# Performance work log

Hardware: AMD Instinct MI355X
Metric: run time of the kernel (lower is better)

The kernel has to match this reference:

```python
import jax, jax.numpy as jnp
import numpy as np

# --- config constants (from init_kwargs) ---
ALPHA = 0.05; SIGMA = 0.2; THETA = 0.3; A = 0.02; B_PAR = 0.1; RHO = 0.5
MULT = 2.0          # config.x_range_final[1]
GAMMA = 0.5         # power-utility exponent: u(x,r)=r*x^g/g, ux=r*x^(g-1)
N_STEPS = 100; T_FINAL = 1.0; DT = T_FINAL / N_STEPS
HID = 64; BATCH = 16384
PEN_SCALE = 100.0; LOWER = 1e-6


def _mlp(W1, b1, W2, b2, W3, b3, s):
    # tiny FeedForwardSubNet: 3 -> HID -> HID -> 1, tanh activations
    h = jnp.tanh(s @ W1 + b1)
    h = jnp.tanh(h @ W2 + b2)
    return h @ W3 + b3


def _penalise(v):
    # penalise_range(v, lower): quadratic hinge below `lower`
    return PEN_SCALE * jnp.square(jnp.maximum(LOWER - v, 0.0))


def setup_inputs() -> dict:
    key = jax.random.key(0)
    ks = jax.random.split(key, 16)
    dw = jax.random.normal(ks[0], (BATCH, 1, N_STEPS), dtype=jnp.float32) * float(np.sqrt(DT))
    X0 = jnp.ones((1,), jnp.float32)
    R0 = jnp.ones((1,), jnp.float32)
    def w(k, shape, fan):
        return jax.random.normal(k, shape, jnp.float32) / np.float32(np.sqrt(fan))
    inp = {"dw": dw, "X0": X0, "R0": R0,
           "pW1": w(ks[1], (3, HID), 3), "pb1": jnp.zeros((HID,), jnp.float32),
           "pW2": w(ks[2], (HID, HID), HID), "pb2": jnp.zeros((HID,), jnp.float32),
           "pW3": w(ks[3], (HID, 1), HID), "pb3": jnp.zeros((1,), jnp.float32),
           "qW1": w(ks[4], (3, HID), 3), "qb1": jnp.zeros((HID,), jnp.float32),
           "qW2": w(ks[5], (HID, HID), HID), "qb2": jnp.zeros((HID,), jnp.float32),
           "qW3": w(ks[6], (HID, 1), HID), "qb3": jnp.zeros((1,), jnp.float32)}
    return inp


def reference(dw, X0, R0, pW1, pb1, pW2, pb2, pW3, pb3, qW1, qb1, qW2, qb2, qW3, qb3):
    Bn = dw.shape[0]
    ones = jnp.ones((Bn, 1), dw.dtype)
    times = jnp.arange(N_STEPS + 1, dtype=dw.dtype) * DT   # [N+1]
    x0 = ones * X0
    R0v = ones * R0
    b_eff = float(np.sign(RHO)) * B_PAR

    # p_0 and dp_0 = d p_0 / d x (per-sample, rowwise independent net)
    def p_of_x(xx):
        st = jnp.concatenate([MULT * times[0] * ones, xx, R0v], 1)
        return _mlp(pW1, pb1, pW2, pb2, pW3, pb3, st)
    p0, p_vjp = jax.vjp(p_of_x, x0)
    (dp0,) = p_vjp(jnp.ones_like(p0))
    pi0 = _mlp(qW1, qb1, qW2, qb2, qW3, qb3,
               jnp.concatenate([MULT * times[0] * ones, x0, R0v], 1))

    dw_t = jnp.transpose(dw, (2, 0, 1))          # [N, B, 1]
    upd = jnp.arange(N_STEPS) < (N_STEPS - 1)    # pi not updated at last step

    def step(carry, inp):
        x, min_x, W, pi = carry
        dwi, t_next, u = inp
        x = x + x * ALPHA * DT + pi * SIGMA * THETA * DT + pi * SIGMA * dwi
        min_x = jnp.minimum(x, min_x)
        W = W + dwi
        Rv = R0v * jnp.exp((A - 0.5 * b_eff ** 2) * t_next + b_eff * W)
        p = p0 * jnp.exp(-(ALPHA + 0.5 * THETA ** 2) * t_next - THETA * W)
        st = jnp.concatenate([MULT * t_next * jnp.ones_like(x), x, Rv], 1)
        pi_new = _mlp(qW1, qb1, qW2, qb2, qW3, qb3, st)
        pi = jnp.where(u, pi_new, pi)
        return (x, min_x, W, pi), (x, Rv, pi, -p)

    (xf, min_x, Wf, pif), (xs, Rs, pis, dMs) = jax.lax.scan(
        step, (x0, x0, jnp.zeros_like(x0), pi0), (dw_t, times[1:], upd))

    # stacked process data, matching tf.concat-over-axis-0 ordering: [(N+1)*B, 1]
    x_all  = jnp.concatenate([x0[None], xs], 0).reshape(-1, 1)
    r_all  = jnp.concatenate([R0v[None], Rs], 0).reshape(-1, 1)
    pi_all = jnp.concatenate([pi0[None], pis], 0).reshape(-1, 1)
    dM_all = jnp.concatenate([(-p0)[None], dMs], 0).reshape(-1, 1)
    dM2_all = jnp.tile(-dp0, (N_STEPS + 1, 1))
    proc = jnp.concatenate([x_all, r_all, pi_all, dM_all, dM2_all], 1)  # [(N+1)*B, 5]

    # losses (non_concave = False branch)
    p_fin = -dMs[-1]
    R_fin = Rs[-1]
    xc = jnp.maximum(xf, LOWER)
    ux = R_fin * xc ** (GAMMA - 1.0)
    u_val = R_fin * xc ** GAMMA / GAMMA
    pen = _penalise(min_x)
    loss_p = jnp.mean(jnp.square(p_fin + ux) + pen)
    loss_pi = loss_p + jnp.mean(-u_val + pen)

    return jnp.concatenate([proc.reshape(-1), jnp.stack([loss_p, loss_pi])])
```

## Files before the change

### kernel.cpp

```cpp
#include <hip/hip_runtime.h>
#include <hip/hip_bf16.h>
#include <math.h>

#define NSTEP 100
#define BATCH 16384
#define MB 16
#define NBLK (BATCH/MB)
#define NT 64

#define C_ALPHA 0.05f
#define C_SIGMA 0.2f
#define C_THETA 0.3f
#define C_DT    0.01f
#define C_LOWER 1e-6f
#define C_PEN   100.0f
#define LOG2E   1.4426950408889634f
#define TSCALE  (2.0f * LOG2E)
#define CRT ( 0.015f * C_DT * LOG2E)
#define CRW ( 0.1f * LOG2E)
#define CPT (-0.095f * C_DT * LOG2E)
#define CPW (-0.3f * LOG2E)

typedef __attribute__((ext_vector_type(8))) short bf16x8;
typedef __attribute__((ext_vector_type(4))) float f32x4;

__device__ __forceinline__ float tanh_pre(float zs) {
    float e = __builtin_amdgcn_exp2f(zs);
    return 1.0f - 2.0f * __builtin_amdgcn_rcpf(e + 1.0f);
}
__device__ __forceinline__ unsigned f2bf_u(float f) {
    unsigned u = __float_as_uint(f);
    return (u + 0x7FFFu + ((u >> 16) & 1u)) >> 16;
}
__device__ __forceinline__ unsigned pack_bf16(float a, float b) {
    union { __hip_bfloat162 h; unsigned u; } cv;
    cv.h = __float22bfloat162_rn(make_float2(a, b));
    return cv.u;
}
__device__ __forceinline__ float dpp_row_sum16(float v) {
    int t;
    t = __builtin_amdgcn_update_dpp(0, __float_as_int(v), 0x128, 0xF, 0xF, true);
    v += __int_as_float(t);
    t = __builtin_amdgcn_update_dpp(0, __float_as_int(v), 0x124, 0xF, 0xF, true);
    v += __int_as_float(t);
    t = __builtin_amdgcn_update_dpp(0, __float_as_int(v), 0x122, 0xF, 0xF, true);
    v += __int_as_float(t);
    t = __builtin_amdgcn_update_dpp(0, __float_as_int(v), 0x121, 0xF, 0xF, true);
    v += __int_as_float(t);
    return v;
}

__global__ __launch_bounds__(NT, 1) void fused_kernel(
        const float* __restrict__ dw, const float* __restrict__ X0,
        const float* __restrict__ R0,
        const float* __restrict__ pW1, const float* __restrict__ pb1,
        const float* __restrict__ pW2, const float* __restrict__ pb2,
        const float* __restrict__ pW3, const float* __restrict__ pb3,
        const float* __restrict__ qW1, const float* __restrict__ qb1,
        const float* __restrict__ qW2, const float* __restrict__ qb2,
        const float* __restrict__ qW3, const float* __restrict__ qb3,
        float* __restrict__ ws, float* __restrict__ out) {
    __shared__ __align__(16) unsigned short sW2T[64 * 72];
    __shared__ __align__(16) float sdw[MB * NSTEP];

    const int lane = threadIdx.x;
    const int b0 = blockIdx.x * MB;
    const int l15 = lane & 15, quad = lane >> 4;

    {
        const float4* g = (const float4*)(dw + (size_t)b0 * NSTEP);
        float4* s = (float4*)sdw;
        #pragma unroll
        for (int u = lane; u < MB * NSTEP / 4; u += NT) s[u] = g[u];
    }
    #pragma unroll 8
    for (int t = 0; t < 64; t++)
        sW2T[lane * 72 + t] = (unsigned short)f2bf_u(qW2[t * 64 + lane] * TSCALE);
    __syncthreads();

    bf16x8 Bf[4][2];
    #pragma unroll
    for (int nt = 0; nt < 4; nt++) {
        const unsigned short* r = &sW2T[(nt * 16 + l15) * 72 + quad * 8];
        Bf[nt][0] = *(const bf16x8*)r;
        Bf[nt][1] = *(const bf16x8*)(r + 32);
    }
    float tco[16], w1xs[16], w1rs[16], b1s[16];
    #pragma unroll
    for (int idx = 0; idx < 16; idx++) {
        int k = (idx < 8) ? (quad * 8 + idx) : (32 + quad * 8 + (idx - 8));
        tco[idx]  = qW1[k] * (2.0f * C_DT * TSCALE);
        w1xs[idx] = qW1[64 + k] * TSCALE;
        w1rs[idx] = qW1[128 + k] * TSCALE;
        b1s[idx]  = qb1[k] * TSCALE;
    }
    float b2v[4], w3v[4];
    #pragma unroll
    for (int nt = 0; nt < 4; nt++) {
        b2v[nt] = qb2[nt * 16 + l15] * TSCALE;
        w3v[nt] = qW3[nt * 16 + l15];
    }
    const float b3 = qb3[0];
    const float X0v = X0[0], R0s = R0[0];
    const int bperm_idx = (((l15 >> 2) * 16) + (l15 & 3)) * 4;

    float p0, dp0;
    {
        float pre = fmaf(pW1[64 + lane], X0v, fmaf(pW1[128 + lane], R0s, pb1[lane]));
        float h1 = tanh_pre(TSCALE * pre);
        float d1 = (1.0f - h1 * h1) * pW1[64 + lane];
        float a0 = pb2[lane], a1 = 0.f, a2 = 0.f, a3 = 0.f;
        float e0 = 0.f, e1 = 0.f, e2 = 0.f, e3 = 0.f;
        for (int i2 = 0; i2 < 64; i2 += 4) {
            float w0 = pW2[(i2 + 0) * 64 + lane];
            float w1 = pW2[(i2 + 1) * 64 + lane];
            float w2 = pW2[(i2 + 2) * 64 + lane];
            float w3 = pW2[(i2 + 3) * 64 + lane];
            a0 = fmaf(__shfl(h1, i2 + 0), w0, a0); e0 = fmaf(__shfl(d1, i2 + 0), w0, e0);
            a1 = fmaf(__shfl(h1, i2 + 1), w1, a1); e1 = fmaf(__shfl(d1, i2 + 1), w1, e1);
            a2 = fmaf(__shfl(h1, i2 + 2), w2, a2); e2 = fmaf(__shfl(d1, i2 + 2), w2, e2);
            a3 = fmaf(__shfl(h1, i2 + 3), w3, a3); e3 = fmaf(__shfl(d1, i2 + 3), w3, e3);
        }
        float pre2 = (a0 + a1) + (a2 + a3);
        float dpre2 = (e0 + e1) + (e2 + e3);
        float h2 = tanh_pre(TSCALE * pre2);
        float d2 = (1.0f - h2 * h2) * dpre2;
        float c1 = h2 * pW3[lane], c2 = d2 * pW3[lane];
        #pragma unroll
        for (int o = 1; o < 64; o <<= 1) {
            c1 += __shfl_xor(c1, o);
            c2 += __shfl_xor(c2, o);
        }
        p0 = c1 + pb3[0]; dp0 = c2;
    }

    auto qnet = [&](float fi, float xv, float rv) -> float {
        union { bf16x8 v; unsigned u[4]; } A0, A1;
        #pragma unroll
        for (int p = 0; p < 8; p++) {
            const int i0 = 2 * p, i1 = 2 * p + 1;
            float z0 = fmaf(w1rs[i0], rv, fmaf(w1xs[i0], xv, fmaf(tco[i0], fi, b1s[i0])));
            float z1 = fmaf(w1rs[i1], rv, fmaf(w1xs[i1], xv, fmaf(tco[i1], fi, b1s[i1])));
            unsigned pk = pack_bf16(tanh_pre(z0), tanh_pre(z1));
            if (p < 4) A0.u[p] = pk; else A1.u[p - 4] = pk;
        }
        f32x4 acc0 = {b2v[0], b2v[0], b2v[0], b2v[0]};
        f32x4 acc1 = {b2v[1], b2v[1], b2v[1], b2v[1]};
        f32x4 acc2 = {b2v[2], b2v[2], b2v[2], b2v[2]};
        f32x4 acc3 = {b2v[3], b2v[3], b2v[3], b2v[3]};
        acc0 = __builtin_amdgcn_mfma_f32_16x16x32_bf16(A0.v, Bf[0][0], acc0, 0, 0, 0);
        acc1 = __builtin_amdgcn_mfma_f32_16x16x32_bf16(A0.v, Bf[1][0], acc1, 0, 0, 0);
        acc2 = __builtin_amdgcn_mfma_f32_16x16x32_bf16(A0.v, Bf[2][0], acc2, 0, 0, 0);
        acc3 = __builtin_amdgcn_mfma_f32_16x16x32_bf16(A0.v, Bf[3][0], acc3, 0, 0, 0);
        acc0 = __builtin_amdgcn_mfma_f32_16x16x32_bf16(A1.v, Bf[0][1], acc0, 0, 0, 0);
        acc1 = __builtin_amdgcn_mfma_f32_16x16x32_bf16(A1.v, Bf[1][1], acc1, 0, 0, 0);
        acc2 = __builtin_amdgcn_mfma_f32_16x16x32_bf16(A1.v, Bf[2][1], acc2, 0, 0, 0);
        acc3 = __builtin_amdgcn_mfma_f32_16x16x32_bf16(A1.v, Bf[3][1], acc3, 0, 0, 0);
        f32x4 part;
        #pragma unroll
        for (int r = 0; r < 4; r++) {
            float sA = fmaf(tanh_pre(acc1[r]), w3v[1], tanh_pre(acc0[r]) * w3v[0]);
            float sB = fmaf(tanh_pre(acc3[r]), w3v[3], tanh_pre(acc2[r]) * w3v[2]);
            part[r] = dpp_row_sum16(sA + sB);
        }
        float sLo = (lane & 1) ? part[1] : part[0];
        float sHi = (lane & 1) ? part[3] : part[2];
        float sel = (lane & 2) ? sHi : sLo;
        int g = __builtin_amdgcn_ds_bpermute(bperm_idx, __float_as_int(sel));
        return __int_as_float(g) + b3;
    };

    float x = X0v, Wsum = 0.0f, minx = X0v;
    float pi = qnet(0.0f, X0v, R0s);
    if (quad == 0) {
        size_t base = (size_t)(b0 + l15) * 5;
        out[base] = X0v; out[base + 1] = R0s; out[base + 2] = pi;
        out[base + 3] = -p0; out[base + 4] = -dp0;
    }

    float dw_next = sdw[l15 * NSTEP];
    #pragma unroll 1
    for (int i = 0; i < NSTEP - 1; i++) {
        const float fi = (float)(i + 1);
        float dwv = dw_next;
        dw_next = sdw[l15 * NSTEP + i + 1];
        float t = pi * C_SIGMA;
        x = fmaf(x, 1.0f + C_ALPHA * C_DT, fmaf(t, dwv, t * (C_THETA * C_DT)));
        minx = fminf(minx, x);
        Wsum += dwv;
        float R = R0s * __builtin_amdgcn_exp2f(fmaf(CRW, Wsum, CRT * fi));
        float pm = p0 * __builtin_amdgcn_exp2f(fmaf(CPW, Wsum, CPT * fi));
        float pin = qnet(fi, x, R);
        if (quad == 0) {
            size_t base = ((size_t)(i + 1) * BATCH + b0 + l15) * 5;
            out[base] = x; out[base + 1] = R; out[base + 2] = pin;
            out[base + 3] = -pm; out[base + 4] = -dp0;
        }
        pi = pin;
    }

    {
        float dwv = dw_next;
        float t = pi * C_SIGMA;
        x = fmaf(x, 1.0f + C_ALPHA * C_DT, fmaf(t, dwv, t * (C_THETA * C_DT)));
        minx = fminf(minx, x);
        Wsum += dwv;
        float Rf = R0s * __builtin_amdgcn_exp2f(fmaf(CRW, Wsum, CRT * (float)NSTEP));
        float pf = p0 * __builtin_amdgcn_exp2f(fmaf(CPW, Wsum, CPT * (float)NSTEP));
        if (quad == 0) {
            size_t base = ((size_t)NSTEP * BATCH + b0 + l15) * 5;
            out[base] = x; out[base + 1] = Rf; out[base + 2] = pi;
            out[base + 3] = -pf; out[base + 4] = -dp0;
        }
        float xc = fmaxf(x, C_LOWER);
        float ux = Rf * rsqrtf(xc);
        float uval = 2.0f * Rf * sqrtf(xc);
        float d = fmaxf(C_LOWER - minx, 0.0f);
        float pen = C_PEN * d * d;
        float t1 = pf + ux;
        float v1 = dpp_row_sum16(t1 * t1 + pen);
        float v2 = dpp_row_sum16(-uval + pen);
        if (lane == 0) {
            atomicAdd(&ws[3], v1);
            atomicAdd(&ws[4], v2);
            __threadfence();
            int old = atomicAdd((int*)(ws + 5), 1);
            if (old == NBLK - 1) {
                float lp = atomicAdd(&ws[3], 0.0f) * (1.0f / (float)BATCH);
                float lq = atomicAdd(&ws[4], 0.0f) * (1.0f / (float)BATCH);
                out[(size_t)(NSTEP + 1) * BATCH * 5] = lp;
                out[(size_t)(NSTEP + 1) * BATCH * 5 + 1] = lp + lq;
            }
        }
    }
}

extern "C" void kernel_launch(void* const* d_in, const int* in_sizes, int n_in,
                              void* d_out, int out_size, void* d_ws, size_t ws_size,
                              hipStream_t stream) {
    const float* dw  = (const float*)d_in[0];
    const float* X0  = (const float*)d_in[1];
    const float* R0  = (const float*)d_in[2];
    const float* pW1 = (const float*)d_in[3];
    const float* pb1 = (const float*)d_in[4];
    const float* pW2 = (const float*)d_in[5];
    const float* pb2 = (const float*)d_in[6];
    const float* pW3 = (const float*)d_in[7];
    const float* pb3 = (const float*)d_in[8];
    const float* qW1 = (const float*)d_in[9];
    const float* qb1 = (const float*)d_in[10];
    const float* qW2 = (const float*)d_in[11];
    const float* qb2 = (const float*)d_in[12];
    const float* qW3 = (const float*)d_in[13];
    const float* qb3 = (const float*)d_in[14];
    float* out = (float*)d_out;
    float* ws  = (float*)d_ws;

    hipMemsetAsync(d_ws, 0, 64, stream);
    fused_kernel<<<NBLK, NT, 0, stream>>>(dw, X0, R0, pW1, pb1, pW2, pb2, pW3, pb3,
                                          qW1, qb1, qW2, qb2, qW3, qb3, ws, out);
}
```

Measured before the change: 209.6 us.

## Split each block's q-net hidden units across two waves with LDS exchange

```diff
diff --git a/kernel.cpp b/kernel.cpp
--- a/kernel.cpp
+++ b/kernel.cpp
@@ -6,7 +6,7 @@
 #define BATCH 16384
 #define MB 16
 #define NBLK (BATCH/MB)
-#define NT 64
+#define NT 128
 
 #define C_ALPHA 0.05f
 #define C_SIGMA 0.2f
@@ -50,7 +50,7 @@
     return v;
 }
 
-__global__ __launch_bounds__(NT, 1) void fused_kernel(
+__global__ __launch_bounds__(NT, 2) void fused_kernel(
         const float* __restrict__ dw, const float* __restrict__ X0,
         const float* __restrict__ R0,
         const float* __restrict__ pW1, const float* __restrict__ pb1,
@@ -62,8 +62,12 @@
         float* __restrict__ ws, float* __restrict__ out) {
     __shared__ __align__(16) unsigned short sW2T[64 * 72];
     __shared__ __align__(16) float sdw[MB * NSTEP];
-
-    const int lane = threadIdx.x;
+    __shared__ __align__(16) uint4 sA[2][2][64];
+    __shared__ __align__(16) float sP[2][2][16];
+
+    const int tid = threadIdx.x;
+    const int lane = tid & 63;
+    const int wv = tid >> 6;
     const int b0 = blockIdx.x * MB;
     const int l15 = lane & 15, quad = lane >> 4;
 
@@ -71,38 +75,38 @@
         const float4* g = (const float4*)(dw + (size_t)b0 * NSTEP);
         float4* s = (float4*)sdw;
         #pragma unroll
-        for (int u = lane; u < MB * NSTEP / 4; u += NT) s[u] = g[u];
-    }
-    #pragma unroll 8
-    for (int t = 0; t < 64; t++)
-        sW2T[lane * 72 + t] = (unsigned short)f2bf_u(qW2[t * 64 + lane] * TSCALE);
+        for (int u = tid; u < MB * NSTEP / 4; u += NT) s[u] = g[u];
+    }
+    for (int u = tid; u < 4096; u += NT) {
+        int k = u >> 6, n = u & 63;
+        sW2T[n * 72 + k] = (unsigned short)f2bf_u(qW2[u] * TSCALE);
+    }
     __syncthreads();
 
-    bf16x8 Bf[4][2];
+    bf16x8 Bf[2][2];
     #pragma unroll
-    for (int nt = 0; nt < 4; nt++) {
-        const unsigned short* r = &sW2T[(nt * 16 + l15) * 72 + quad * 8];
-        Bf[nt][0] = *(const bf16x8*)r;
-        Bf[nt][1] = *(const bf16x8*)(r + 32);
-    }
-    float tco[16], w1xs[16], w1rs[16], b1s[16];
+    for (int t = 0; t < 2; t++) {
+        const unsigned short* r = &sW2T[(wv * 32 + t * 16 + l15) * 72 + quad * 8];
+        Bf[t][0] = *(const bf16x8*)r;
+        Bf[t][1] = *(const bf16x8*)(r + 32);
+    }
+    float tco[8], w1xs[8], w1rs[8], b1s[8];
     #pragma unroll
-    for (int idx = 0; idx < 16; idx++) {
-        int k = (idx < 8) ? (quad * 8 + idx) : (32 + quad * 8 + (idx - 8));
-        tco[idx]  = qW1[k] * (2.0f * C_DT * TSCALE);
-        w1xs[idx] = qW1[64 + k] * TSCALE;
-        w1rs[idx] = qW1[128 + k] * TSCALE;
-        b1s[idx]  = qb1[k] * TSCALE;
-    }
-    float b2v[4], w3v[4];
+    for (int j = 0; j < 8; j++) {
+        int k = wv * 32 + quad * 8 + j;
+        tco[j]  = qW1[k] * (2.0f * C_DT * TSCALE);
+        w1xs[j] = qW1[64 + k] * TSCALE;
+        w1rs[j] = qW1[128 + k] * TSCALE;
+        b1s[j]  = qb1[k] * TSCALE;
+    }
+    float b2v[2], w3v[2];
     #pragma unroll
-    for (int nt = 0; nt < 4; nt++) {
-        b2v[nt] = qb2[nt * 16 + l15] * TSCALE;
-        w3v[nt] = qW3[nt * 16 + l15];
+    for (int t = 0; t < 2; t++) {
+        b2v[t] = qb2[wv * 32 + t * 16 + l15] * TSCALE;
+        w3v[t] = qW3[wv * 32 + t * 16 + l15];
     }
     const float b3 = qb3[0];
     const float X0v = X0[0], R0s = R0[0];
-    const int bperm_idx = (((l15 >> 2) * 16) + (l15 & 3)) * 4;
 
     float p0, dp0;
     {
@@ -134,45 +138,39 @@
         p0 = c1 + pb3[0]; dp0 = c2;
     }
 
-    auto qnet = [&](float fi, float xv, float rv) -> float {
-        union { bf16x8 v; unsigned u[4]; } A0, A1;
-        #pragma unroll
-        for (int p = 0; p < 8; p++) {
+    auto qnet = [&](int par, float fi, float xv, float rv) -> float {
+        union { uint4 u4; bf16x8 v; unsigned u[4]; } Aloc, Aoth;
+        #pragma unroll
+        for (int p = 0; p < 4; p++) {
             const int i0 = 2 * p, i1 = 2 * p + 1;
             float z0 = fmaf(w1rs[i0], rv, fmaf(w1xs[i0], xv, fmaf(tco[i0], fi, b1s[i0])));
             float z1 = fmaf(w1rs[i1], rv, fmaf(w1xs[i1], xv, fmaf(tco[i1], fi, b1s[i1])));
-            unsigned pk = pack_bf16(tanh_pre(z0), tanh_pre(z1));
-            if (p < 4) A0.u[p] = pk; else A1.u[p - 4] = pk;
-        }
+            Aloc.u[p] = pack_bf16(tanh_pre(z0), tanh_pre(z1));
+        }
+        sA[par][wv][lane] = Aloc.u4;
+        __syncthreads();
+        Aoth.u4 = sA[par][1 - wv][lane];
+        bf16x8 A0 = (wv == 0) ? Aloc.v : Aoth.v;
+        bf16x8 A1 = (wv == 0) ? Aoth.v : Aloc.v;
         f32x4 acc0 = {b2v[0], b2v[0], b2v[0], b2v[0]};
         f32x4 acc1 = {b2v[1], b2v[1], b2v[1], b2v[1]};
-        f32x4 acc2 = {b2v[2], b2v[2], b2v[2], b2v[2]};
-        f32x4 acc3 = {b2v[3], b2v[3], b2v[3], b2v[3]};
-        acc0 = __builtin_amdgcn_mfma_f32_16x16x32_bf16(A0.v, Bf[0][0], acc0, 0, 0, 0);
-        acc1 = __builtin_amdgcn_mfma_f32_16x16x32_bf16(A0.v, Bf[1][0], acc1, 0, 0, 0);
-        acc2 = __builtin_amdgcn_mfma_f32_16x16x32_bf16(A0.v, Bf[2][0], acc2, 0, 0, 0);
-        acc3 = __builtin_amdgcn_mfma_f32_16x16x32_bf16(A0.v, Bf[3][0], acc3, 0, 0, 0);
-        acc0 = __builtin_amdgcn_mfma_f32_16x16x32_bf16(A1.v, Bf[0][1], acc0, 0, 0, 0);
-        acc1 = __builtin_amdgcn_mfma_f32_16x16x32_bf16(A1.v, Bf[1][1], acc1, 0, 0, 0);
-        acc2 = __builtin_amdgcn_mfma_f32_16x16x32_bf16(A1.v, Bf[2][1], acc2, 0, 0, 0);
-        acc3 = __builtin_amdgcn_mfma_f32_16x16x32_bf16(A1.v, Bf[3][1], acc3, 0, 0, 0);
+        acc0 = __builtin_amdgcn_mfma_f32_16x16x32_bf16(A0, Bf[0][0], acc0, 0, 0, 0);
+        acc1 = __builtin_amdgcn_mfma_f32_16x16x32_bf16(A0, Bf[1][0], acc1, 0, 0, 0);
+        acc0 = __builtin_amdgcn_mfma_f32_16x16x32_bf16(A1, Bf[0][1], acc0, 0, 0, 0);
+        acc1 = __builtin_amdgcn_mfma_f32_16x16x32_bf16(A1, Bf[1][1], acc1, 0, 0, 0);
         f32x4 part;
         #pragma unroll
-        for (int r = 0; r < 4; r++) {
-            float sA = fmaf(tanh_pre(acc1[r]), w3v[1], tanh_pre(acc0[r]) * w3v[0]);
-            float sB = fmaf(tanh_pre(acc3[r]), w3v[3], tanh_pre(acc2[r]) * w3v[2]);
-            part[r] = dpp_row_sum16(sA + sB);
-        }
-        float sLo = (lane & 1) ? part[1] : part[0];
-        float sHi = (lane & 1) ? part[3] : part[2];
-        float sel = (lane & 2) ? sHi : sLo;
-        int g = __builtin_amdgcn_ds_bpermute(bperm_idx, __float_as_int(sel));
-        return __int_as_float(g) + b3;
+        for (int r = 0; r < 4; r++)
+            part[r] = dpp_row_sum16(
+                fmaf(tanh_pre(acc1[r]), w3v[1], tanh_pre(acc0[r]) * w3v[0]));
+        if (l15 == 0) *(f32x4*)&sP[par][wv][quad * 4] = part;
+        __syncthreads();
+        return sP[par][0][l15] + sP[par][1][l15] + b3;
     };
 
     float x = X0v, Wsum = 0.0f, minx = X0v;
-    float pi = qnet(0.0f, X0v, R0s);
-    if (quad == 0) {
+    float pi = qnet(0, 0.0f, X0v, R0s);
+    if (wv == 1 && quad == 0) {
         size_t base = (size_t)(b0 + l15) * 5;
         out[base] = X0v; out[base + 1] = R0s; out[base + 2] = pi;
         out[base + 3] = -p0; out[base + 4] = -dp0;
@@ -190,8 +188,8 @@
         Wsum += dwv;
         float R = R0s * __builtin_amdgcn_exp2f(fmaf(CRW, Wsum, CRT * fi));
         float pm = p0 * __builtin_amdgcn_exp2f(fmaf(CPW, Wsum, CPT * fi));
-        float pin = qnet(fi, x, R);
-        if (quad == 0) {
+        float pin = qnet((i + 1) & 1, fi, x, R);
+        if (wv == 1 && quad == 0) {
             size_t base = ((size_t)(i + 1) * BATCH + b0 + l15) * 5;
             out[base] = x; out[base + 1] = R; out[base + 2] = pin;
             out[base + 3] = -pm; out[base + 4] = -dp0;
@@ -207,29 +205,31 @@
         Wsum += dwv;
         float Rf = R0s * __builtin_amdgcn_exp2f(fmaf(CRW, Wsum, CRT * (float)NSTEP));
         float pf = p0 * __builtin_amdgcn_exp2f(fmaf(CPW, Wsum, CPT * (float)NSTEP));
-        if (quad == 0) {
+        if (wv == 1 && quad == 0) {
             size_t base = ((size_t)NSTEP * BATCH + b0 + l15) * 5;
             out[base] = x; out[base + 1] = Rf; out[base + 2] = pi;
             out[base + 3] = -pf; out[base + 4] = -dp0;
         }
-        float xc = fmaxf(x, C_LOWER);
-        float ux = Rf * rsqrtf(xc);
-        float uval = 2.0f * Rf * sqrtf(xc);
-        float d = fmaxf(C_LOWER - minx, 0.0f);
-        float pen = C_PEN * d * d;
-        float t1 = pf + ux;
-        float v1 = dpp_row_sum16(t1 * t1 + pen);
-        float v2 = dpp_row_sum16(-uval + pen);
-        if (lane == 0) {
-            atomicAdd(&ws[3], v1);
-            atomicAdd(&ws[4], v2);
-            __threadfence();
-            int old = atomicAdd((int*)(ws + 5), 1);
-            if (old == NBLK - 1) {
-                float lp = atomicAdd(&ws[3], 0.0f) * (1.0f / (float)BATCH);
-                float lq = atomicAdd(&ws[4], 0.0f) * (1.0f / (float)BATCH);
-                out[(size_t)(NSTEP + 1) * BATCH * 5] = lp;
-                out[(size_t)(NSTEP + 1) * BATCH * 5 + 1] = lp + lq;
+        if (wv == 0) {
+            float xc = fmaxf(x, C_LOWER);
+            float ux = Rf * rsqrtf(xc);
+            float uval = 2.0f * Rf * sqrtf(xc);
+            float d = fmaxf(C_LOWER - minx, 0.0f);
+            float pen = C_PEN * d * d;
+            float t1 = pf + ux;
+            float v1 = dpp_row_sum16(t1 * t1 + pen);
+            float v2 = dpp_row_sum16(-uval + pen);
+            if (lane == 0) {
+                atomicAdd(&ws[3], v1);
+                atomicAdd(&ws[4], v2);
+                __threadfence();
+                int old = atomicAdd((int*)(ws + 5), 1);
+                if (old == NBLK - 1) {
+                    float lp = atomicAdd(&ws[3], 0.0f) * (1.0f / (float)BATCH);
+                    float lq = atomicAdd(&ws[4], 0.0f) * (1.0f / (float)BATCH);
+                    out[(size_t)(NSTEP + 1) * BATCH * 5] = lp;
+                    out[(size_t)(NSTEP + 1) * BATCH * 5 + 1] = lp + lq;
+                }
             }
         }
     }
```

Result: no change. 208.9 us (-0.3%).

## Precompute R and p paths off the serial loop and shorten per-step dependency chain

Applied to the files above, without the earlier changes.

```diff
diff --git a/kernel.cpp b/kernel.cpp
--- a/kernel.cpp
+++ b/kernel.cpp
@@ -20,6 +20,7 @@
 #define CRW ( 0.1f * LOG2E)
 #define CPT (-0.095f * C_DT * LOG2E)
 #define CPW (-0.3f * LOG2E)
+#define XMUL (1.0f + C_ALPHA * C_DT)
 
 typedef __attribute__((ext_vector_type(8))) short bf16x8;
 typedef __attribute__((ext_vector_type(4))) float f32x4;
@@ -62,6 +63,8 @@
         float* __restrict__ ws, float* __restrict__ out) {
     __shared__ __align__(16) unsigned short sW2T[64 * 72];
     __shared__ __align__(16) float sdw[MB * NSTEP];
+    __shared__ __align__(16) float sR[NSTEP * MB];
+    __shared__ float sPf[MB];
 
     const int lane = threadIdx.x;
     const int b0 = blockIdx.x * MB;
@@ -78,31 +81,8 @@
         sW2T[lane * 72 + t] = (unsigned short)f2bf_u(qW2[t * 64 + lane] * TSCALE);
     __syncthreads();
 
-    bf16x8 Bf[4][2];
-    #pragma unroll
-    for (int nt = 0; nt < 4; nt++) {
-        const unsigned short* r = &sW2T[(nt * 16 + l15) * 72 + quad * 8];
-        Bf[nt][0] = *(const bf16x8*)r;
-        Bf[nt][1] = *(const bf16x8*)(r + 32);
-    }
-    float tco[16], w1xs[16], w1rs[16], b1s[16];
-    #pragma unroll
-    for (int idx = 0; idx < 16; idx++) {
-        int k = (idx < 8) ? (quad * 8 + idx) : (32 + quad * 8 + (idx - 8));
-        tco[idx]  = qW1[k] * (2.0f * C_DT * TSCALE);
-        w1xs[idx] = qW1[64 + k] * TSCALE;
-        w1rs[idx] = qW1[128 + k] * TSCALE;
-        b1s[idx]  = qb1[k] * TSCALE;
-    }
-    float b2v[4], w3v[4];
-    #pragma unroll
-    for (int nt = 0; nt < 4; nt++) {
-        b2v[nt] = qb2[nt * 16 + l15] * TSCALE;
-        w3v[nt] = qW3[nt * 16 + l15];
-    }
+    const float X0v = X0[0], R0s = R0[0];
     const float b3 = qb3[0];
-    const float X0v = X0[0], R0s = R0[0];
-    const int bperm_idx = (((l15 >> 2) * 16) + (l15 & 3)) * 4;
 
     float p0, dp0;
     {
@@ -134,34 +114,91 @@
         p0 = c1 + pb3[0]; dp0 = c2;
     }
 
-    auto qnet = [&](float fi, float xv, float rv) -> float {
-        union { bf16x8 v; unsigned u[4]; } A0, A1;
-        #pragma unroll
-        for (int p = 0; p < 8; p++) {
-            const int i0 = 2 * p, i1 = 2 * p + 1;
-            float z0 = fmaf(w1rs[i0], rv, fmaf(w1xs[i0], xv, fmaf(tco[i0], fi, b1s[i0])));
-            float z1 = fmaf(w1rs[i1], rv, fmaf(w1xs[i1], xv, fmaf(tco[i1], fi, b1s[i1])));
-            unsigned pk = pack_bf16(tanh_pre(z0), tanh_pre(z1));
-            if (p < 4) A0.u[p] = pk; else A1.u[p - 4] = pk;
-        }
+    {
+        const int ps = lane >> 2;
+        const int pc = lane & 3;
+        float loc = 0.0f;
+        #pragma unroll 5
+        for (int j = pc * 25; j < pc * 25 + 25; j++) loc += sdw[ps * NSTEP + j];
+        float o0 = __shfl(loc, ps * 4 + 0);
+        float o1 = __shfl(loc, ps * 4 + 1);
+        float o2 = __shfl(loc, ps * 4 + 2);
+        float W = 0.0f;
+        if (pc > 0) W += o0;
+        if (pc > 1) W += o1;
+        if (pc > 2) W += o2;
+        #pragma unroll 5
+        for (int t = pc * 25 + 1; t <= pc * 25 + 25; t++) {
+            W += sdw[ps * NSTEP + (t - 1)];
+            float ft = (float)t;
+            float R = R0s * __builtin_amdgcn_exp2f(fmaf(CRW, W, CRT * ft));
+            float pm = p0 * __builtin_amdgcn_exp2f(fmaf(CPW, W, CPT * ft));
+            sR[(t - 1) * MB + ps] = R;
+            size_t base = ((size_t)t * BATCH + b0 + ps) * 5;
+            out[base + 1] = R; out[base + 3] = -pm; out[base + 4] = -dp0;
+            if (t == NSTEP) sPf[ps] = pm;
+        }
+        if (lane < MB) {
+            size_t base = (size_t)(b0 + lane) * 5;
+            out[base] = X0v; out[base + 1] = R0s;
+            out[base + 3] = -p0; out[base + 4] = -dp0;
+        }
+    }
+    __syncthreads();
+
+    bf16x8 Bf[4][2];
+    #pragma unroll
+    for (int nt = 0; nt < 4; nt++) {
+        const unsigned short* r = &sW2T[(nt * 16 + l15) * 72 + quad * 8];
+        Bf[nt][0] = *(const bf16x8*)r;
+        Bf[nt][1] = *(const bf16x8*)(r + 32);
+    }
+    float tco[16], w1xs[16], w1rs[16], zc[16];
+    #pragma unroll
+    for (int idx = 0; idx < 16; idx++) {
+        int k = (idx < 8) ? (quad * 8 + idx) : (32 + quad * 8 + (idx - 8));
+        tco[idx]  = qW1[k] * (2.0f * C_DT * TSCALE);
+        w1xs[idx] = qW1[64 + k] * TSCALE;
+        w1rs[idx] = qW1[128 + k] * TSCALE;
+        zc[idx]   = qb1[k] * TSCALE;
+    }
+    float b2v[4], w3v[4];
+    #pragma unroll
+    for (int nt = 0; nt < 4; nt++) {
+        b2v[nt] = qb2[nt * 16 + l15] * TSCALE;
+        w3v[nt] = qW3[nt * 16 + l15];
+    }
+    const int bperm_idx = (((l15 >> 2) * 16) + (l15 & 3)) * 4;
+
+    auto l23 = [&](const bf16x8& A0, const bf16x8& A1) -> float {
         f32x4 acc0 = {b2v[0], b2v[0], b2v[0], b2v[0]};
         f32x4 acc1 = {b2v[1], b2v[1], b2v[1], b2v[1]};
         f32x4 acc2 = {b2v[2], b2v[2], b2v[2], b2v[2]};
         f32x4 acc3 = {b2v[3], b2v[3], b2v[3], b2v[3]};
-        acc0 = __builtin_amdgcn_mfma_f32_16x16x32_bf16(A0.v, Bf[0][0], acc0, 0, 0, 0);
-        acc1 = __builtin_amdgcn_mfma_f32_16x16x32_bf16(A0.v, Bf[1][0], acc1, 0, 0, 0);
-        acc2 = __builtin_amdgcn_mfma_f32_16x16x32_bf16(A0.v, Bf[2][0], acc2, 0, 0, 0);
-        acc3 = __builtin_amdgcn_mfma_f32_16x16x32_bf16(A0.v, Bf[3][0], acc3, 0, 0, 0);
-        acc0 = __builtin_amdgcn_mfma_f32_16x16x32_bf16(A1.v, Bf[0][1], acc0, 0, 0, 0);
-        acc1 = __builtin_amdgcn_mfma_f32_16x16x32_bf16(A1.v, Bf[1][1], acc1, 0, 0, 0);
-        acc2 = __builtin_amdgcn_mfma_f32_16x16x32_bf16(A1.v, Bf[2][1], acc2, 0, 0, 0);
-        acc3 = __builtin_amdgcn_mfma_f32_16x16x32_bf16(A1.v, Bf[3][1], acc3, 0, 0, 0);
+        acc0 = __builtin_amdgcn_mfma_f32_16x16x32_bf16(A0, Bf[0][0], acc0, 0, 0, 0);
+        acc1 = __builtin_amdgcn_mfma_f32_16x16x32_bf16(A0, Bf[1][0], acc1, 0, 0, 0);
+        acc2 = __builtin_amdgcn_mfma_f32_16x16x32_bf16(A0, Bf[2][0], acc2, 0, 0, 0);
+        acc3 = __builtin_amdgcn_mfma_f32_16x16x32_bf16(A0, Bf[3][0], acc3, 0, 0, 0);
+        acc0 = __builtin_amdgcn_mfma_f32_16x16x32_bf16(A1, Bf[0][1], acc0, 0, 0, 0);
+        acc1 = __builtin_amdgcn_mfma_f32_16x16x32_bf16(A1, Bf[1][1], acc1, 0, 0, 0);
+        acc2 = __builtin_amdgcn_mfma_f32_16x16x32_bf16(A1, Bf[2][1], acc2, 0, 0, 0);
+        acc3 = __builtin_amdgcn_mfma_f32_16x16x32_bf16(A1, Bf[3][1], acc3, 0, 0, 0);
+        float th[16];
+        #pragma unroll
+        for (int r = 0; r < 4; r++) {
+            th[r]      = tanh_pre(acc0[r]);
+            th[4 + r]  = tanh_pre(acc1[r]);
+            th[8 + r]  = tanh_pre(acc2[r]);
+            th[12 + r] = tanh_pre(acc3[r]);
+        }
         f32x4 part;
         #pragma unroll
         for (int r = 0; r < 4; r++) {
-            float sA = fmaf(tanh_pre(acc1[r]), w3v[1], tanh_pre(acc0[r]) * w3v[0]);
-            float sB = fmaf(tanh_pre(acc3[r]), w3v[3], tanh_pre(acc2[r]) * w3v[2]);
-            part[r] = dpp_row_sum16(sA + sB);
+            float s = th[r] * w3v[0];
+            s = fmaf(th[4 + r],  w3v[1], s);
+            s = fmaf(th[8 + r],  w3v[2], s);
+            s = fmaf(th[12 + r], w3v[3], s);
+            part[r] = dpp_row_sum16(s);
         }
         float sLo = (lane & 1) ? part[1] : part[0];
         float sHi = (lane & 1) ? part[3] : part[2];
@@ -170,48 +207,72 @@
         return __int_as_float(g) + b3;
     };
 
-    float x = X0v, Wsum = 0.0f, minx = X0v;
-    float pi = qnet(0.0f, X0v, R0s);
-    if (quad == 0) {
-        size_t base = (size_t)(b0 + l15) * 5;
-        out[base] = X0v; out[base + 1] = R0s; out[base + 2] = pi;
-        out[base + 3] = -p0; out[base + 4] = -dp0;
-    }
-
-    float dw_next = sdw[l15 * NSTEP];
+    float pi;
+    {
+        union { bf16x8 v; unsigned u[4]; } A0, A1;
+        float z[16];
+        #pragma unroll
+        for (int idx = 0; idx < 16; idx++)
+            z[idx] = fmaf(w1rs[idx], R0s, fmaf(w1xs[idx], X0v, zc[idx]));
+        float th[16];
+        #pragma unroll
+        for (int idx = 0; idx < 16; idx++) th[idx] = tanh_pre(z[idx]);
+        #pragma unroll
+        for (int p = 0; p < 4; p++) {
+            A0.u[p] = pack_bf16(th[2 * p], th[2 * p + 1]);
+            A1.u[p] = pack_bf16(th[8 + 2 * p], th[9 + 2 * p]);
+        }
+        pi = l23(A0.v, A1.v);
+    }
+    if (quad == 0) out[(size_t)(b0 + l15) * 5 + 2] = pi;
+
+    float x = X0v, minx = X0v;
+    float dw_cur = sdw[l15 * NSTEP];
+    float R_cur = sR[l15];
+    float* po = out + ((size_t)BATCH + b0 + l15) * 5;
+
     #pragma unroll 1
     for (int i = 0; i < NSTEP - 1; i++) {
-        const float fi = (float)(i + 1);
-        float dwv = dw_next;
-        dw_next = sdw[l15 * NSTEP + i + 1];
-        float t = pi * C_SIGMA;
-        x = fmaf(x, 1.0f + C_ALPHA * C_DT, fmaf(t, dwv, t * (C_THETA * C_DT)));
+        float dw_nx = sdw[l15 * NSTEP + i + 1];
+        float R_nx  = sR[(i + 1) * MB + l15];
+        float rz[16];
+        #pragma unroll
+        for (int idx = 0; idx < 16; idx++) {
+            zc[idx] += tco[idx];
+            rz[idx] = fmaf(w1rs[idx], R_cur, zc[idx]);
+        }
+        float xa = x * XMUL;
+        float cdw = fmaf(C_SIGMA, dw_cur, C_SIGMA * C_THETA * C_DT);
+        x = fmaf(pi, cdw, xa);
         minx = fminf(minx, x);
-        Wsum += dwv;
-        float R = R0s * __builtin_amdgcn_exp2f(fmaf(CRW, Wsum, CRT * fi));
-        float pm = p0 * __builtin_amdgcn_exp2f(fmaf(CPW, Wsum, CPT * fi));
-        float pin = qnet(fi, x, R);
-        if (quad == 0) {
-            size_t base = ((size_t)(i + 1) * BATCH + b0 + l15) * 5;
-            out[base] = x; out[base + 1] = R; out[base + 2] = pin;
-            out[base + 3] = -pm; out[base + 4] = -dp0;
-        }
+        if (quad == 0) po[0] = x;
+        float z[16];
+        #pragma unroll
+        for (int idx = 0; idx < 16; idx++) z[idx] = fmaf(w1xs[idx], x, rz[idx]);
+        float th[16];
+        #pragma unroll
+        for (int idx = 0; idx < 16; idx++) th[idx] = tanh_pre(z[idx]);
+        union { bf16x8 v; unsigned u[4]; } A0, A1;
+        #pragma unroll
+        for (int p = 0; p < 4; p++) {
+            A0.u[p] = pack_bf16(th[2 * p], th[2 * p + 1]);
+            A1.u[p] = pack_bf16(th[8 + 2 * p], th[9 + 2 * p]);
+        }
+        float pin = l23(A0.v, A1.v);
+        if (quad == 0) po[2] = pin;
         pi = pin;
-    }
-
-    {
-        float dwv = dw_next;
-        float t = pi * C_SIGMA;
-        x = fmaf(x, 1.0f + C_ALPHA * C_DT, fmaf(t, dwv, t * (C_THETA * C_DT)));
+        dw_cur = dw_nx; R_cur = R_nx;
+        po += (size_t)BATCH * 5;
+    }
+
+    {
+        float xa = x * XMUL;
+        float cdw = fmaf(C_SIGMA, dw_cur, C_SIGMA * C_THETA * C_DT);
+        x = fmaf(pi, cdw, xa);
         minx = fminf(minx, x);
-        Wsum += dwv;
-        float Rf = R0s * __builtin_amdgcn_exp2f(fmaf(CRW, Wsum, CRT * (float)NSTEP));
-        float pf = p0 * __builtin_amdgcn_exp2f(fmaf(CPW, Wsum, CPT * (float)NSTEP));
-        if (quad == 0) {
-            size_t base = ((size_t)NSTEP * BATCH + b0 + l15) * 5;
-            out[base] = x; out[base + 1] = Rf; out[base + 2] = pi;
-            out[base + 3] = -pf; out[base + 4] = -dp0;
-        }
+        float Rf = R_cur;
+        float pf = sPf[l15];
+        if (quad == 0) { po[0] = x; po[2] = pi; }
         float xc = fmaxf(x, C_LOWER);
         float ux = Rf * rsqrtf(xc);
         float uval = 2.0f * Rf * sqrtf(xc);
```

Measured after the change: 217.3 us. 1.04x slower.
